# Kernel tuning notes

Measured on AMD Instinct MI355X. Metric: run time of the kernel, lower is better.

The kernel has to match this reference:

```python
import jax, jax.numpy as jnp
import numpy as np

N_HEADS = 16
NEG = -1e9  # matches torch masked_fill value


def setup_inputs() -> dict:
    key = jax.random.key(0)
    ks = jax.random.split(key, 8)
    B, S, E = 4, 1024, 1024
    x = jax.random.normal(ks[0], (B, S, E), dtype=jnp.float32)
    event_lengths = jax.random.randint(ks[1], (B,), 1, S + 1)
    scale = 1.0 / np.sqrt(E)
    Wq = jax.random.normal(ks[2], (E, E), dtype=jnp.float32) * scale
    bq = jnp.zeros((E,), dtype=jnp.float32)
    Wk = jax.random.normal(ks[3], (E, E), dtype=jnp.float32) * scale
    bk = jnp.zeros((E,), dtype=jnp.float32)
    Wv = jax.random.normal(ks[4], (E, E), dtype=jnp.float32) * scale
    bv = jnp.zeros((E,), dtype=jnp.float32)
    return {"x": x, "Wq": Wq, "bq": bq, "Wk": Wk, "bk": bk,
            "Wv": Wv, "bv": bv, "event_lengths": event_lengths}


def reference(x, Wq, bq, Wk, bk, Wv, bv, event_lengths):
    B, S, E = x.shape
    H = N_HEADS
    D = E // H
    # fused projections, then split heads: [B,S,E] -> [B,H,S,D]
    def split(t):
        return t.reshape(B, S, H, D).transpose(0, 2, 1, 3)
    q = split(x @ Wq + bq)
    k = split(x @ Wk + bk)
    v = split(x @ Wv + bv)
    scores = jnp.einsum('bhsd,bhtd->bhst', q, k) / jnp.sqrt(jnp.float32(D))
    # rectangular length mask: valid iff row < len AND col < len
    idx = jnp.arange(S)
    valid = idx[None, :] < event_lengths[:, None]           # [B,S]
    mask = valid[:, :, None] & valid[:, None, :]            # [B,S,S]
    scores = jnp.where(mask[:, None, :, :], scores, NEG)
    attn = jax.nn.softmax(scores, axis=-1)
    out = jnp.einsum('bhst,bhtd->bhsd', attn, v)            # [B,H,S,D]
    # concat heads (== torch.cat over head outputs); NOTE: summarize proj is
    # dead code in the original (its result is overwritten), dropout is eval-identity
    return out.transpose(0, 2, 1, 3).reshape(B, S, E)
```

## Files before the change

kernel.cpp:

```cpp
#include <hip/hip_runtime.h>
#include <stdint.h>


using u16     = unsigned short;
using half8   = __attribute__((ext_vector_type(8))) _Float16;
using floatx4 = __attribute__((ext_vector_type(4))) float;

#define MFMA16(a, b, c) __builtin_amdgcn_mfma_f32_16x16x32_f16(a, b, c, 0, 0, 0)

__device__ __forceinline__ u16 f2h(float f) {
  _Float16 h = (_Float16)f; u16 u; __builtin_memcpy(&u, &h, 2); return u;
}

template <int CTRL>
__device__ __forceinline__ float dppf(float v) {
  return __int_as_float(__builtin_amdgcn_update_dpp(
      0, __float_as_int(v), CTRL, 0xF, 0xF, true));
}
__device__ __forceinline__ float rowsum16(float v) {
  v += dppf<0x121>(v);
  v += dppf<0x122>(v);
  v += dppf<0x124>(v);
  v += dppf<0x128>(v);
  return v;
}

__device__ __forceinline__ void async_cp16(void* lds, const void* g) {
  __builtin_amdgcn_global_load_lds(
      (__attribute__((address_space(1))) uint32_t*)(uintptr_t)g,
      (__attribute__((address_space(3))) uint32_t*)(uint32_t)(uintptr_t)lds,
      16, 0, 0);
}

__global__ void k_prep(const float* __restrict__ x, u16* __restrict__ xh,
                       const float* __restrict__ w0, const float* __restrict__ w1,
                       const float* __restrict__ w2,
                       u16* __restrict__ o0, u16* __restrict__ o1,
                       u16* __restrict__ o2, float* __restrict__ vsum) {
  __shared__ float t[32][33];
  const int bx = blockIdx.x;
  if (bx < 4096) {
    int i = (bx * 256 + threadIdx.x) * 4;
    float4 v = *(const float4*)(x + i);
    ushort4 hv;
    hv.x = f2h(v.x);
    hv.y = f2h(v.y);
    hv.z = f2h(v.z);
    hv.w = f2h(v.w);
    *(ushort4*)(xh + i) = hv;
    if (bx == 0) {
      float4 z = {0.f, 0.f, 0.f, 0.f};
#pragma unroll
      for (int e = 0; e < 4; e++) ((float4*)vsum)[threadIdx.x * 4 + e] = z;
    }
    return;
  }
  const int id = bx - 4096;
  const int z = id >> 10, rem = id & 1023;
  const float* W = z == 0 ? w0 : (z == 1 ? w1 : w2);
  u16* oh = z == 0 ? o0 : (z == 1 ? o1 : o2);
  const int kb = (rem & 31) * 32, nb = (rem >> 5) * 32;
  const int tx = threadIdx.x & 31, ty = threadIdx.x >> 5;
  for (int r = ty; r < 32; r += 8) t[r][tx] = W[(kb + r) * 1024 + nb + tx];
  __syncthreads();
  for (int r = ty; r < 32; r += 8)
    oh[(nb + r) * 1024 + kb + tx] = f2h(t[tx][r]);
}

__launch_bounds__(256, 4)
__global__ void k_proj(const u16* __restrict__ xh,
                       const u16* __restrict__ wqT, const u16* __restrict__ wkT,
                       const u16* __restrict__ wvT,
                       const float* __restrict__ bq, const float* __restrict__ bk,
                       const float* __restrict__ bv,
                       u16* __restrict__ qh, u16* __restrict__ kh,
                       u16* __restrict__ vth, float* __restrict__ vsum) {
  __shared__ u16 Sm[17408];
  const int z = blockIdx.z;
  const u16* wT = z == 0 ? wqT : (z == 1 ? wkT : wvT);
  const float* bias = z == 0 ? bq : (z == 1 ? bk : bv);
  u16* oh = z == 0 ? qh : (z == 1 ? kh : vth);
  const float oscale = (z == 0) ? 0.18033688011112042f : 1.0f;

  const int tid = threadIdx.x, l = tid & 63, w = tid >> 6;
  const int quad = l >> 4, col = l & 15;
  const int m0 = blockIdx.x * 128, n0 = blockIdx.y * 128;
  const int wm = (w & 1) * 64, wn = (w >> 1) * 64;

  const int row0 = tid >> 3, ch = tid & 7;
  const int sc8 = (ch ^ (row0 & 7)) * 8;
  int gofs[4], lofs[4];
#pragma unroll
  for (int p = 0; p < 4; p++) {
    gofs[p] = (row0 + 32 * p) * 1024 + sc8;
    lofs[p] = (tid + p * 256) * 8;
  }

  const u16* Ag = xh + m0 * 1024;
  const u16* Bg = wT + n0 * 1024;

  int ar[2][4], br[2][4];
#pragma unroll
  for (int ks = 0; ks < 2; ks++) {
#pragma unroll
    for (int i = 0; i < 4; i++) {
      int r = wm + i * 16 + col;
      ar[ks][i] = r * 64 + (((ks * 4 + quad) ^ (r & 7)) * 8);
    }
#pragma unroll
    for (int j = 0; j < 4; j++) {
      int r = wn + j * 16 + col;
      br[ks][j] = r * 64 + (((ks * 4 + quad) ^ (r & 7)) * 8);
    }
  }

  floatx4 zero4 = {0.f, 0.f, 0.f, 0.f};
  floatx4 acc[4][4];
#pragma unroll
  for (int i = 0; i < 4; i++)
#pragma unroll
    for (int j = 0; j < 4; j++) acc[i][j] = zero4;

  for (int k0 = 0; k0 < 1024; k0 += 64) {
    __syncthreads();
#pragma unroll
    for (int p = 0; p < 4; p++) async_cp16(Sm + lofs[p], Ag + gofs[p] + k0);
#pragma unroll
    for (int p = 0; p < 4; p++)
      async_cp16(Sm + 8192 + lofs[p], Bg + gofs[p] + k0);
    __syncthreads();

#pragma unroll
    for (int ks = 0; ks < 2; ks++) {
      half8 fa[4], fb[4];
#pragma unroll
      for (int i = 0; i < 4; i++) fa[i] = *(const half8*)(Sm + ar[ks][i]);
#pragma unroll
      for (int j = 0; j < 4; j++)
        fb[j] = *(const half8*)(Sm + 8192 + br[ks][j]);
#pragma unroll
      for (int i = 0; i < 4; i++)
#pragma unroll
        for (int j = 0; j < 4; j++) acc[i][j] = MFMA16(fa[i], fb[j], acc[i][j]);
    }
  }

  const int bidx = m0 >> 10;
  const int sbase = m0 & 1023;
  __syncthreads();

#pragma unroll
  for (int j = 0; j < 4; j++) {
    int nloc = wn + j * 16 + col;
    float bb = bias[n0 + nloc];
#pragma unroll
    for (int i = 0; i < 4; i++)
#pragma unroll
      for (int r = 0; r < 4; r++) {
        int mloc = wm + i * 16 + quad * 4 + r;
        Sm[mloc * 136 + nloc] = f2h((acc[i][j][r] + bb) * oscale);
      }
  }
  __syncthreads();

  if (z != 2) {
#pragma unroll
    for (int k = 0; k < 8; k++) {
      int c = tid + k * 256;
      int mloc = c >> 4, n = (c & 15) * 8;
      int hh = (n0 + n) >> 6, d = (n0 + n) & 63;
      half8 vv = *(const half8*)(Sm + mloc * 136 + n);
      *(half8*)(oh + ((bidx * 16 + hh) * 1024 + sbase + mloc) * 64 + d) = vv;
    }
  } else {
#pragma unroll
    for (int k = 0; k < 8; k++) {
      int c = tid + k * 256;
      int nloc = c & 127, s0 = (c >> 7) * 8;
      int hh = (n0 + nloc) >> 6, d = (n0 + nloc) & 63;
      u16 tmp[8];
#pragma unroll
      for (int e = 0; e < 8; e++) tmp[e] = Sm[(s0 + e) * 136 + nloc];
      *(half8*)(vth + ((bidx * 16 + hh) * 64 + d) * 1024 + sbase + s0) =
          *(half8*)tmp;
    }
#pragma unroll
    for (int j = 0; j < 4; j++) {
      int nloc = wn + j * 16 + col;
      float bb = bias[n0 + nloc];
      float part = 16.0f * bb;
#pragma unroll
      for (int i = 0; i < 4; i++)
#pragma unroll
        for (int r = 0; r < 4; r++) part += acc[i][j][r];
      part += __shfl_xor(part, 16, 64);
      part += __shfl_xor(part, 32, 64);
      if (quad == 0) {
        int hh = (n0 + nloc) >> 6, d = (n0 + nloc) & 63;
        unsafeAtomicAdd(vsum + (bidx * 16 + hh) * 64 + d, part);
      }
    }
  }
}

__device__ __forceinline__ void stage64(u16* lds, const u16* g, int row_stride,
                                        int tid) {
#pragma unroll
  for (int p = 0; p < 2; p++) {
    int slot = (p * 256 + tid) * 8;
    int row = slot >> 6;
    int gp = (slot >> 3) & 7;
    int gl = gp ^ (row & 7);
    async_cp16(lds + slot, g + row * row_stride + gl * 8);
  }
}

__launch_bounds__(256)
__global__ void k_attn(const u16* __restrict__ qh_g,
                       const u16* __restrict__ kh_g,
                       const u16* __restrict__ vth_g,
                       const float* __restrict__ vsum, const int* __restrict__ elen,
                       float* __restrict__ out) {
  __shared__ u16 QP[4096];
  __shared__ u16 Bufs[2][8192];
  const int tid = threadIdx.x, l = tid & 63, w = tid >> 6;
  const int quad = l >> 4, col = l & 15;
  const int id = blockIdx.x;
  const int b = (id + (id >> 8)) & 3;
  const int h = (id >> 2) & 15;
  const int bh = b * 16 + h;
  const int q0 = ((id >> 6) & 15) * 64;
  const int len = elen[b];

  if (q0 >= len) {
    float val = vsum[bh * 64 + l] * (1.0f / 1024.0f);
    float* op = out + (b * 1024 + q0) * 1024 + h * 64 + l;
    for (int r = w; r < 64; r += 4) op[r * 1024] = val;
    return;
  }

  const u16* kh_b  = kh_g + bh * 65536;
  const u16* vth_b = vth_g + bh * 65536;

  stage64(QP, qh_g + (bh * 1024 + q0) * 64, 64, tid);
  stage64(Bufs[0], kh_b, 64, tid);
  stage64(Bufs[0] + 4096, vth_b, 1024, tid);
  __syncthreads();

  half8 qf[2];
  {
    int qrow = w * 16 + col;
#pragma unroll
    for (int ks = 0; ks < 2; ks++)
      qf[ks] = *(const half8*)(QP + qrow * 64 +
                               (((ks * 4 + quad) ^ (qrow & 7)) * 8));
  }

  int kvo[2][4];
#pragma unroll
  for (int ks = 0; ks < 2; ks++)
#pragma unroll
    for (int j = 0; j < 4; j++) {
      int n = j * 16 + col;
      kvo[ks][j] = n * 64 + (((ks * 4 + quad) ^ (n & 7)) * 8);
    }
  int p_rd[2];
#pragma unroll
  for (int ks = 0; ks < 2; ks++) {
    int row = w * 16 + col;
    p_rd[ks] = row * 64 + (((ks * 4 + quad) ^ (row & 7)) * 8);
  }
  int p_wr[4][4];
#pragma unroll
  for (int r = 0; r < 4; r++) {
    int row = w * 16 + quad * 4 + r;
#pragma unroll
    for (int j = 0; j < 4; j++) {
      int cj = j * 2 + (col >> 3);
      p_wr[r][j] = row * 64 + ((cj ^ (row & 7)) * 8) + (col & 7);
    }
  }

  floatx4 zero4 = {0.f, 0.f, 0.f, 0.f};
  floatx4 O[4];
  float lp[4];
#pragma unroll
  for (int j = 0; j < 4; j++) O[j] = zero4;
#pragma unroll
  for (int r = 0; r < 4; r++) lp[r] = 0.f;

  const int ntt = (len + 63) >> 6;
  for (int tt = 0; tt < ntt; ++tt) {
    const int t0 = tt * 64;
    u16* cur = Bufs[tt & 1];
    if (tt + 1 < ntt) {
      u16* nxt = Bufs[(tt + 1) & 1];
      const int t1 = t0 + 64;
      stage64(nxt, kh_b + t1 * 64, 64, tid);
      stage64(nxt + 4096, vth_b + t1, 1024, tid);
    }

    floatx4 sc[4];
#pragma unroll
    for (int j = 0; j < 4; j++) sc[j] = zero4;
#pragma unroll
    for (int ks = 0; ks < 2; ks++) {
#pragma unroll
      for (int j = 0; j < 4; j++) {
        half8 kb = *(const half8*)(cur + kvo[ks][j]);
        sc[j] = MFMA16(qf[ks], kb, sc[j]);
      }
    }

    if (t0 + 64 > len) {
#pragma unroll
      for (int j = 0; j < 4; j++) {
        bool inv = (t0 + j * 16 + col) >= len;
#pragma unroll
        for (int r = 0; r < 4; r++)
          if (inv) sc[j][r] = -3e38f;
      }
    }

#pragma unroll
    for (int r = 0; r < 4; r++) {
#pragma unroll
      for (int j = 0; j < 4; j++) {
        float e = __builtin_exp2f(sc[j][r]);
        QP[p_wr[r][j]] = f2h(e);
        lp[r] += e;
      }
    }

#pragma unroll
    for (int ks = 0; ks < 2; ks++) {
      half8 pa = *(const half8*)(QP + p_rd[ks]);
#pragma unroll
      for (int j = 0; j < 4; j++) {
        half8 vb = *(const half8*)(cur + 4096 + kvo[ks][j]);
        O[j] = MFMA16(pa, vb, O[j]);
      }
    }

    __syncthreads();
  }

  float l_r[4];
#pragma unroll
  for (int r = 0; r < 4; r++) l_r[r] = rowsum16(lp[r]);
#pragma unroll
  for (int r = 0; r < 4; r++) {
    int s = q0 + w * 16 + quad * 4 + r;
    float invl = 1.0f / l_r[r];
    bool valid = (s < len);
#pragma unroll
    for (int j = 0; j < 4; j++) {
      int d = j * 16 + col;
      float val = valid ? O[j][r] * invl : vsum[bh * 64 + d] * (1.0f / 1024.0f);
      out[(b * 1024 + s) * 1024 + h * 64 + d] = val;
    }
  }
}

extern "C" void kernel_launch(void* const* d_in, const int* in_sizes, int n_in,
                              void* d_out, int out_size, void* d_ws, size_t ws_size,
                              hipStream_t stream) {
  (void)in_sizes; (void)n_in; (void)out_size; (void)ws_size;
  const float* x  = (const float*)d_in[0];
  const float* Wq = (const float*)d_in[1];
  const float* bq = (const float*)d_in[2];
  const float* Wk = (const float*)d_in[3];
  const float* bk = (const float*)d_in[4];
  const float* Wv = (const float*)d_in[5];
  const float* bv = (const float*)d_in[6];
  const int* elen = (const int*)d_in[7];
  float* out = (float*)d_out;

  char* ws = (char*)d_ws;
  const size_t MB = 1024 * 1024;
  u16* xh  = (u16*)(ws + 0 * MB);
  u16* wqT = (u16*)(ws + 8 * MB);
  u16* wkT = (u16*)(ws + 10 * MB);
  u16* wvT = (u16*)(ws + 12 * MB);
  u16* qh  = (u16*)(ws + 14 * MB);
  u16* kh  = (u16*)(ws + 22 * MB);
  u16* vth = (u16*)(ws + 30 * MB);
  float* vsum = (float*)(ws + 38 * MB);

  k_prep<<<7168, 256, 0, stream>>>(x, xh, Wq, Wk, Wv, wqT, wkT, wvT, vsum);
  k_proj<<<dim3(32, 8, 3), 256, 0, stream>>>(xh, wqT, wkT, wvT, bq, bk, bv,
                                             qh, kh, vth, vsum);
  k_attn<<<1024, 256, 0, stream>>>(qh, kh, vth, vsum, elen, out);
}
```

Baseline: 152.7 us.

## Compute transposed score tiles so each warp owns key rows, pack P stores

```diff
diff --git a/kernel.cpp b/kernel.cpp
--- a/kernel.cpp
+++ b/kernel.cpp
@@ -10,19 +10,6 @@
 
 __device__ __forceinline__ u16 f2h(float f) {
   _Float16 h = (_Float16)f; u16 u; __builtin_memcpy(&u, &h, 2); return u;
-}
-
-template <int CTRL>
-__device__ __forceinline__ float dppf(float v) {
-  return __int_as_float(__builtin_amdgcn_update_dpp(
-      0, __float_as_int(v), CTRL, 0xF, 0xF, true));
-}
-__device__ __forceinline__ float rowsum16(float v) {
-  v += dppf<0x121>(v);
-  v += dppf<0x122>(v);
-  v += dppf<0x124>(v);
-  v += dppf<0x128>(v);
-  return v;
 }
 
 __device__ __forceinline__ void async_cp16(void* lds, const void* g) {
@@ -247,15 +234,22 @@
   stage64(Bufs[0] + 4096, vth_b, 1024, tid);
   __syncthreads();
 
-  half8 qf[2];
-  {
-    int qrow = w * 16 + col;
+  half8 qf[4][2];
+#pragma unroll
+  for (int jq = 0; jq < 4; jq++) {
+    int qrow = jq * 16 + col;
 #pragma unroll
     for (int ks = 0; ks < 2; ks++)
-      qf[ks] = *(const half8*)(QP + qrow * 64 +
-                               (((ks * 4 + quad) ^ (qrow & 7)) * 8));
-  }
-
+      qf[jq][ks] = *(const half8*)(QP + qrow * 64 +
+                                   (((ks * 4 + quad) ^ (qrow & 7)) * 8));
+  }
+
+  int ko[2];
+#pragma unroll
+  for (int ks = 0; ks < 2; ks++) {
+    int r = w * 16 + col;
+    ko[ks] = r * 64 + (((ks * 4 + quad) ^ (r & 7)) * 8);
+  }
   int kvo[2][4];
 #pragma unroll
   for (int ks = 0; ks < 2; ks++)
@@ -264,20 +258,13 @@
       int n = j * 16 + col;
       kvo[ks][j] = n * 64 + (((ks * 4 + quad) ^ (n & 7)) * 8);
     }
-  int p_rd[2];
-#pragma unroll
-  for (int ks = 0; ks < 2; ks++) {
-    int row = w * 16 + col;
-    p_rd[ks] = row * 64 + (((ks * 4 + quad) ^ (row & 7)) * 8);
-  }
-  int p_wr[4][4];
-#pragma unroll
-  for (int r = 0; r < 4; r++) {
-    int row = w * 16 + quad * 4 + r;
-#pragma unroll
-    for (int j = 0; j < 4; j++) {
-      int cj = j * 2 + (col >> 3);
-      p_wr[r][j] = row * 64 + ((cj ^ (row & 7)) * 8) + (col & 7);
+  int p_wr[4];
+  {
+    int chv = w * 2 + (quad >> 1);
+#pragma unroll
+    for (int jq = 0; jq < 4; jq++) {
+      int row = jq * 16 + col;
+      p_wr[jq] = row * 64 + ((chv ^ (row & 7)) * 8) + (quad & 1) * 4;
     }
   }
 
@@ -287,7 +274,7 @@
 #pragma unroll
   for (int j = 0; j < 4; j++) O[j] = zero4;
 #pragma unroll
-  for (int r = 0; r < 4; r++) lp[r] = 0.f;
+  for (int jq = 0; jq < 4; jq++) lp[jq] = 0.f;
 
   const int ntt = (len + 63) >> 6;
   for (int tt = 0; tt < ntt; ++tt) {
@@ -302,39 +289,44 @@
 
     floatx4 sc[4];
 #pragma unroll
-    for (int j = 0; j < 4; j++) sc[j] = zero4;
+    for (int jq = 0; jq < 4; jq++) sc[jq] = zero4;
 #pragma unroll
     for (int ks = 0; ks < 2; ks++) {
-#pragma unroll
-      for (int j = 0; j < 4; j++) {
-        half8 kb = *(const half8*)(cur + kvo[ks][j]);
-        sc[j] = MFMA16(qf[ks], kb, sc[j]);
+      half8 kf = *(const half8*)(cur + ko[ks]);
+#pragma unroll
+      for (int jq = 0; jq < 4; jq++) sc[jq] = MFMA16(kf, qf[jq][ks], sc[jq]);
+    }
+
+    if (t0 + 64 > len) {
+#pragma unroll
+      for (int r = 0; r < 4; r++) {
+        bool inv = (t0 + w * 16 + quad * 4 + r) >= len;
+#pragma unroll
+        for (int jq = 0; jq < 4; jq++)
+          if (inv) sc[jq][r] = -3e38f;
       }
     }
 
-    if (t0 + 64 > len) {
-#pragma unroll
-      for (int j = 0; j < 4; j++) {
-        bool inv = (t0 + j * 16 + col) >= len;
-#pragma unroll
-        for (int r = 0; r < 4; r++)
-          if (inv) sc[j][r] = -3e38f;
-      }
-    }
-
-#pragma unroll
-    for (int r = 0; r < 4; r++) {
-#pragma unroll
-      for (int j = 0; j < 4; j++) {
-        float e = __builtin_exp2f(sc[j][r]);
-        QP[p_wr[r][j]] = f2h(e);
-        lp[r] += e;
-      }
-    }
+#pragma unroll
+    for (int jq = 0; jq < 4; jq++) {
+      float e0 = __builtin_exp2f(sc[jq][0]);
+      float e1 = __builtin_exp2f(sc[jq][1]);
+      float e2 = __builtin_exp2f(sc[jq][2]);
+      float e3 = __builtin_exp2f(sc[jq][3]);
+      lp[jq] += (e0 + e1) + (e2 + e3);
+      uint2 pk;
+      pk.x = (uint32_t)f2h(e0) | ((uint32_t)f2h(e1) << 16);
+      pk.y = (uint32_t)f2h(e2) | ((uint32_t)f2h(e3) << 16);
+      *(uint2*)(QP + p_wr[jq]) = pk;
+    }
+
+    asm volatile("s_waitcnt lgkmcnt(0)" ::: "memory");
+    __builtin_amdgcn_s_barrier();
+    __builtin_amdgcn_sched_barrier(0);
 
 #pragma unroll
     for (int ks = 0; ks < 2; ks++) {
-      half8 pa = *(const half8*)(QP + p_rd[ks]);
+      half8 pa = *(const half8*)(QP + ko[ks]);
 #pragma unroll
       for (int j = 0; j < 4; j++) {
         half8 vb = *(const half8*)(cur + 4096 + kvo[ks][j]);
@@ -345,13 +337,27 @@
     __syncthreads();
   }
 
-  float l_r[4];
-#pragma unroll
-  for (int r = 0; r < 4; r++) l_r[r] = rowsum16(lp[r]);
+  float* lred = (float*)Bufs;
+#pragma unroll
+  for (int jq = 0; jq < 4; jq++) {
+    float v = lp[jq];
+    v += __shfl_xor(v, 16, 64);
+    v += __shfl_xor(v, 32, 64);
+    lp[jq] = v;
+  }
+  if (quad == 0) {
+#pragma unroll
+    for (int jq = 0; jq < 4; jq++) lred[w * 64 + jq * 16 + col] = lp[jq];
+  }
+  __syncthreads();
+
 #pragma unroll
   for (int r = 0; r < 4; r++) {
-    int s = q0 + w * 16 + quad * 4 + r;
-    float invl = 1.0f / l_r[r];
+    int qloc = w * 16 + quad * 4 + r;
+    int s = q0 + qloc;
+    float lr = (lred[qloc] + lred[64 + qloc]) +
+               (lred[128 + qloc] + lred[192 + qloc]);
+    float invl = 1.0f / lr;
     bool valid = (s < len);
 #pragma unroll
     for (int j = 0; j < 4; j++) {
```

Measured after the change: 152.2 us. No clear change (-0.4%).
